# Optimization experiments

Hardware: AMD Instinct MI355X
Metric: run time of the kernel (lower is better)

Reference implementation:

```python
import jax, jax.numpy as jnp
import numpy as np

EPS = 1e-5

def _conv1x1_bn(x, W, b, g, beta):
    # 1x1 conv == channel matmul; BN in training mode uses batch stats over (N,H,W)
    y = jnp.einsum('bchw,oc->bohw', x, W) + b[None, :, None, None]
    mu = jnp.mean(y, axis=(0, 2, 3))
    var = jnp.var(y, axis=(0, 2, 3))
    y = (y - mu[None, :, None, None]) * jax.lax.rsqrt(var + EPS)[None, :, None, None]
    return y * g[None, :, None, None] + beta[None, :, None, None]


def setup_inputs() -> dict:
    key = jax.random.key(0)
    ks = jax.random.split(key, 7)
    b, c, h, w = 8, 256, 64, 64
    sc = 1.0 / np.sqrt(c)
    inp = {
        'x': jax.random.normal(ks[0], (b, c, h, w), jnp.float32),
        'Wq': jax.random.normal(ks[1], (c, c), jnp.float32) * sc,
        'bq': jax.random.normal(ks[2], (c,), jnp.float32) * 0.02,
        'gq': jnp.ones((c,), jnp.float32),
        'betaq': jnp.zeros((c,), jnp.float32),
        'Wk': jax.random.normal(ks[3], (c, c), jnp.float32) * sc,
        'bk': jax.random.normal(ks[4], (c,), jnp.float32) * 0.02,
        'gk': jnp.ones((c,), jnp.float32),
        'betak': jnp.zeros((c,), jnp.float32),
        'Wv': jax.random.normal(ks[5], (c, c), jnp.float32) * sc,
        'bv': jax.random.normal(ks[6], (c,), jnp.float32) * 0.02,
        'gv': jnp.ones((c,), jnp.float32),
        'betav': jnp.zeros((c,), jnp.float32),
    }
    return inp


def reference(x, Wq, bq, gq, betaq, Wk, bk, gk, betak, Wv, bv, gv, betav):
    b, c, h, w = x.shape
    scale = float(h) ** (-0.5)
    Q = _conv1x1_bn(x, Wq, bq, gq, betaq).reshape(b, c, h * w)
    K = _conv1x1_bn(x, Wk, bk, gk, betak).reshape(b, c, h * w)
    V = _conv1x1_bn(x, Wv, bv, gv, betav).reshape(b, c, h * w)
    # un-normalized attention (no softmax)
    pixelMap = jnp.einsum('bcq,bck->bqk', Q, K) * scale  # [b, N, N]
    out = jnp.einsum('bqk,bck->bcq', pixelMap, V)        # [b, c, N]
    return out.reshape(b, c, h, w)
```

## Files before the change

### kernel.cpp

```cpp
#include <hip/hip_runtime.h>
#include <hip/hip_bf16.h>


#define BB 8
#define CC 256
#define NPIX 4096
#define PTOT 32768
#define EPSV 1e-5f
#define SCALEV 0.125f

#define OFF_PG    0L
#define OFF_SP    3145728L
#define OFF_S     3162112L
#define OFF_GHAT  3164160L
#define OFF_XBAR  3229696L
#define OFF_WP    3229952L
#define OFF_WKTF  3426560L
#define OFF_WVTF  3492096L
#define OFF_CVEC  3557632L
#define OFF_U     3558400L
#define OFF_W2    3560448L
#define OFF_HB    3562496L
#define OFF_Y     3564544L
#define OFF_R     3564800L
#define OFF_OFFV  3565056L
#define OFF_GBF   3567104L
#define OFF_WQT   3829248L
#define OFF_WKT   3862016L
#define OFF_WVB   3894784L
#define OFF_ZT    3927552L
#define OFF_FT    3960320L
#define OFF_TBF   4222464L

typedef __attribute__((ext_vector_type(8))) short short8;
typedef __attribute__((ext_vector_type(4))) float f32x4;

#define MFMA16(a, b, c) __builtin_amdgcn_mfma_f32_16x16x32_bf16((a), (b), (c), 0, 0, 0)

__device__ __forceinline__ ushort f2bf(float f) {
    union { float f; unsigned u; } v; v.f = f;
    const unsigned r = (v.u + 0x7FFFu + ((v.u >> 16) & 1u)) >> 16;
    return (ushort)r;
}

__device__ __forceinline__ float bf2f(ushort u) {
    union { unsigned u; float f; } v; v.u = ((unsigned)u) << 16;
    return v.f;
}

__device__ __forceinline__ ushort2 f2bf2(float a, float b) {
    __hip_bfloat162 h = __float22bfloat162_rn(float2{a, b});
    union { __hip_bfloat162 h; ushort2 u; } v; v.h = h;
    return v.u;
}

__device__ __forceinline__ float block_reduce(float v, float* red, int tid) {
    red[tid] = v; __syncthreads();
    for (int st = 128; st > 0; st >>= 1) {
        if (tid < st) red[tid] += red[tid + st];
        __syncthreads();
    }
    float r = red[0]; __syncthreads();
    return r;
}

__global__ __launch_bounds__(256) void gram_mfma(const float* __restrict__ x,
                                                 float* __restrict__ Pg,
                                                 float* __restrict__ Sp) {
    __shared__ __align__(16) ushort Ab[128 * 72];
    __shared__ __align__(16) ushort Bb[128 * 72];
    __shared__ float rs[128];
    const int tid = threadIdx.x;
    const int ks = blockIdx.x, b = blockIdx.y, tt = blockIdx.z;
    const int it = (tt == 1) ? 1 : 0;
    const int jt = (tt == 0) ? 0 : 1;
    const bool diag = (tt < 2);
    const int i0 = it * 128, j0 = jt * 128, k0 = ks * 512;
    const float* xb = x + (long)b * CC * NPIX;
    const int c = tid & 15, rp = tid >> 4;
    const int wave = tid >> 6, lane = tid & 63;
    const int wr = (wave >> 1) * 64, wc = (wave & 1) * 64;
    const int m = lane & 15, q8 = (lane >> 4) * 8;

    if (tid < 128) rs[tid] = 0.f;
    float rloc[8] = {};
    f32x4 acc[4][4];
    #pragma unroll
    for (int a = 0; a < 4; ++a)
        #pragma unroll
        for (int q = 0; q < 4; ++q) acc[a][q] = (f32x4){0.f, 0.f, 0.f, 0.f};

    for (int kc = 0; kc < 512; kc += 64) {
        __syncthreads();
        #pragma unroll
        for (int pp = 0; pp < 8; ++pp) {
            const int row = pp * 16 + rp;
            const float4 v = *(const float4*)&xb[(long)(i0 + row) * NPIX + k0 + kc + c * 4];
            rloc[pp] += v.x + v.y + v.z + v.w;
            const ushort2 w01 = f2bf2(v.x, v.y);
            const ushort2 w23 = f2bf2(v.z, v.w);
            ushort4 w; w.x = w01.x; w.y = w01.y; w.z = w23.x; w.w = w23.y;
            *(ushort4*)&Ab[row * 72 + c * 4] = w;
        }
        if (!diag) {
            #pragma unroll
            for (int pp = 0; pp < 8; ++pp) {
                const int row = pp * 16 + rp;
                const float4 v = *(const float4*)&xb[(long)(j0 + row) * NPIX + k0 + kc + c * 4];
                const ushort2 w01 = f2bf2(v.x, v.y);
                const ushort2 w23 = f2bf2(v.z, v.w);
                ushort4 w; w.x = w01.x; w.y = w01.y; w.z = w23.x; w.w = w23.y;
                *(ushort4*)&Bb[row * 72 + c * 4] = w;
            }
        }
        __syncthreads();
        const ushort* Bsrc = diag ? Ab : Bb;
        #pragma unroll
        for (int kk = 0; kk < 2; ++kk) {
            short8 af[4], bfv[4];
            #pragma unroll
            for (int a = 0; a < 4; ++a)
                af[a] = *(const short8*)&Ab[(wr + a * 16 + m) * 72 + kk * 32 + q8];
            #pragma unroll
            for (int q = 0; q < 4; ++q)
                bfv[q] = *(const short8*)&Bsrc[(wc + q * 16 + m) * 72 + kk * 32 + q8];
            #pragma unroll
            for (int a = 0; a < 4; ++a)
                #pragma unroll
                for (int q = 0; q < 4; ++q)
                    acc[a][q] = MFMA16(af[a], bfv[q], acc[a][q]);
        }
    }
    if (diag) {
        #pragma unroll
        for (int pp = 0; pp < 8; ++pp) atomicAdd(&rs[pp * 16 + rp], rloc[pp]);
        __syncthreads();
        if (tid < 128) Sp[(((long)ks * 8 + b) * 2 + it) * 128 + tid] = rs[tid];
    }
    float* Pt = Pg + (((long)ks * 8 + b) * 3 + tt) * 16384;
    const int rq = (lane >> 4) * 4;
    #pragma unroll
    for (int a = 0; a < 4; ++a) {
        #pragma unroll
        for (int q = 0; q < 4; ++q) {
            const int col = wc + q * 16 + m;
            #pragma unroll
            for (int reg = 0; reg < 4; ++reg)
                Pt[(long)(wr + a * 16 + rq + reg) * 128 + col] = acc[a][q][reg];
        }
    }
}

__global__ __launch_bounds__(256) void reduce_mirror(const float* __restrict__ Pg,
                                                     const float* __restrict__ Sp,
                                                     ushort* __restrict__ Gbf,
                                                     float* __restrict__ Ghat,
                                                     float* __restrict__ S,
                                                     float* __restrict__ xbar) {
    const int blk = blockIdx.x, tid = threadIdx.x;
    if (blk == 48) {
        const int it2 = tid >> 7, rr = tid & 127;
        float xacc = 0.f;
        for (int b = 0; b < BB; ++b) {
            float acc = 0.f;
            #pragma unroll
            for (int ks = 0; ks < 8; ++ks)
                acc += Sp[(((long)ks * 8 + b) * 2 + it2) * 128 + rr];
            S[b * 256 + tid] = acc;
            xacc += acc;
        }
        xbar[tid] = xacc * (1.0f / PTOT);
        return;
    }
    __shared__ float tile[32][33];
    const int tt = blk >> 4, sub = blk & 15;
    const int sr = (sub >> 2) * 32, sc = (sub & 3) * 32;
    const int it = (tt == 1) ? 1 : 0;
    const int jt = (tt == 0) ? 0 : 1;
    const bool offd = (tt == 2);
    const int gi0 = it * 128 + sr, gj0 = jt * 128 + sc;
    const int r = tid >> 3, c4 = (tid & 7) * 4;
    float gh[4] = {0.f, 0.f, 0.f, 0.f};
    for (int b = 0; b < BB; ++b) {
        float s0 = 0.f, s1 = 0.f, s2 = 0.f, s3 = 0.f;
        #pragma unroll
        for (int ks = 0; ks < 8; ++ks) {
            const float4 v = *(const float4*)&Pg[(((long)ks * 8 + b) * 3 + tt) * 16384
                                                 + (long)(sr + r) * 128 + sc + c4];
            s0 += v.x; s1 += v.y; s2 += v.z; s3 += v.w;
        }
        ushort4 w;
        w.x = f2bf(s0); w.y = f2bf(s1); w.z = f2bf(s2); w.w = f2bf(s3);
        *(ushort4*)&Gbf[(long)b * 65536 + (long)(gi0 + r) * 256 + gj0 + c4] = w;
        gh[0] += s0; gh[1] += s1; gh[2] += s2; gh[3] += s3;
        if (offd) {
            tile[r][c4 + 0] = s0; tile[r][c4 + 1] = s1;
            tile[r][c4 + 2] = s2; tile[r][c4 + 3] = s3;
            __syncthreads();
            ushort4 t;
            t.x = f2bf(tile[c4 + 0][r]); t.y = f2bf(tile[c4 + 1][r]);
            t.z = f2bf(tile[c4 + 2][r]); t.w = f2bf(tile[c4 + 3][r]);
            *(ushort4*)&Gbf[(long)b * 65536 + (long)(gj0 + r) * 256 + gi0 + c4] = t;
            __syncthreads();
        }
    }
    float4 g4;
    g4.x = gh[0] * (1.0f / PTOT); g4.y = gh[1] * (1.0f / PTOT);
    g4.z = gh[2] * (1.0f / PTOT); g4.w = gh[3] * (1.0f / PTOT);
    *(float4*)&Ghat[(long)(gi0 + r) * 256 + gj0 + c4] = g4;
    if (offd) {
        tile[r][c4 + 0] = g4.x; tile[r][c4 + 1] = g4.y;
        tile[r][c4 + 2] = g4.z; tile[r][c4 + 3] = g4.w;
        __syncthreads();
        float4 t4;
        t4.x = tile[c4 + 0][r]; t4.y = tile[c4 + 1][r];
        t4.z = tile[c4 + 2][r]; t4.w = tile[c4 + 3][r];
        *(float4*)&Ghat[(long)(gj0 + r) * 256 + gi0 + c4] = t4;
    }
}

__global__ void stats_quad(const float* __restrict__ Wq, const float* __restrict__ Wk,
                           const float* __restrict__ Wv, const float* __restrict__ Ghat,
                           const float* __restrict__ xbar,
                           const float* bq, const float* gq, const float* betaq,
                           const float* bk, const float* gk, const float* betak,
                           const float* bv, const float* gv, const float* betav,
                           float* __restrict__ Wp, float* __restrict__ cvec,
                           ushort* __restrict__ WqT, ushort* __restrict__ WkT,
                           ushort* __restrict__ Wvb, float* __restrict__ WkTf,
                           float* __restrict__ WvTf) {
    const int o = blockIdx.x, t = blockIdx.y, tid = threadIdx.x;
    const float* Wt  = t == 0 ? Wq : (t == 1 ? Wk : Wv);
    const float* bt  = t == 0 ? bq : (t == 1 ? bk : bv);
    const float* gt  = t == 0 ? gq : (t == 1 ? gk : gv);
    const float* bet = t == 0 ? betaq : (t == 1 ? betak : betav);
    __shared__ float wrow[256];
    __shared__ float red[256];
    wrow[tid] = Wt[o * 256 + tid];
    __syncthreads();
    const float* grow = Ghat + (long)tid * 256;
    float tj = 0.f;
    #pragma unroll 8
    for (int k = 0; k < 256; k += 4) {
        const float4 g = *(const float4*)&grow[k];
        tj += g.x * wrow[k] + g.y * wrow[k + 1] + g.z * wrow[k + 2] + g.w * wrow[k + 3];
    }
    const float q2 = block_reduce(wrow[tid] * tj, red, tid);
    const float wx = block_reduce(wrow[tid] * xbar[tid], red, tid);
    const float bo = bt[o];
    const float mu = wx + bo;
    const float var = q2 + 2.f * bo * mu - bo * bo - mu * mu;
    const float a = gt[o] * rsqrtf(var + EPSV);
    const float wpv = a * wrow[tid];
    Wp[(long)t * 65536 + o * 256 + tid] = wpv;
    const ushort wb = f2bf(wpv);
    if (t == 0) {
        WqT[(long)tid * 256 + o] = wb;
    } else if (t == 1) {
        WkT[(long)tid * 256 + o] = wb;
        WkTf[(long)tid * 256 + o] = wpv;
    } else {
        Wvb[(long)o * 256 + tid] = wb;
        WvTf[(long)tid * 256 + o] = wpv;
    }
    if (tid == 0) cvec[t * 256 + o] = a * (bo - mu) + bet[o];
}

__device__ __forceinline__ void gemm_tile(const ushort* __restrict__ Ab,
                                          const ushort* __restrict__ Bb,
                                          ushort* __restrict__ Db,
                                          int m0, int n0, int mode, int bz,
                                          const float* __restrict__ u,
                                          const float* __restrict__ cvec,
                                          const float* __restrict__ r,
                                          const float* __restrict__ hb, int tid) {
    const int wave = tid >> 6, lane = tid & 63;
    const int wr = (wave >> 1) * 64, wc = (wave & 1) * 64;
    const int m = lane & 15, q8 = (lane >> 4) * 8;
    f32x4 acc[4][4];
    #pragma unroll
    for (int a = 0; a < 4; ++a)
        #pragma unroll
        for (int q = 0; q < 4; ++q) acc[a][q] = (f32x4){0.f, 0.f, 0.f, 0.f};
    #pragma unroll
    for (int kk = 0; kk < 8; ++kk) {
        short8 af[4], bfv[4];
        #pragma unroll
        for (int a = 0; a < 4; ++a)
            af[a] = *(const short8*)&Ab[(long)(m0 + wr + a * 16 + m) * 256 + kk * 32 + q8];
        #pragma unroll
        for (int q = 0; q < 4; ++q)
            bfv[q] = *(const short8*)&Bb[(long)(n0 + wc + q * 16 + m) * 256 + kk * 32 + q8];
        #pragma unroll
        for (int a = 0; a < 4; ++a)
            #pragma unroll
            for (int q = 0; q < 4; ++q)
                acc[a][q] = MFMA16(af[a], bfv[q], acc[a][q]);
    }
    const int rq = (lane >> 4) * 4;
    #pragma unroll
    for (int a = 0; a < 4; ++a) {
        #pragma unroll
        for (int q = 0; q < 4; ++q) {
            const int col = n0 + wc + q * 16 + m;
            #pragma unroll
            for (int reg = 0; reg < 4; ++reg) {
                const int row = m0 + wr + a * 16 + rq + reg;
                const float v = acc[a][q][reg];
                if (mode == 0) {
                    Db[(long)col * 256 + row] = f2bf(v);
                } else {
                    const float rv = r[col];
                    const float t2 = hb[bz * 256 + col] + 4096.0f * rv;
                    const float val = SCALEV * (v + u[bz * 256 + row] * rv + cvec[512 + row] * t2);
                    Db[(long)row * 256 + col] = f2bf(val);
                }
            }
        }
    }
}

__global__ __launch_bounds__(256) void zmida(const ushort* __restrict__ WkT,
                                             const ushort* __restrict__ WqT,
                                             ushort* __restrict__ ZT,
                                             const float* __restrict__ Wp,
                                             const float* __restrict__ WkTf,
                                             const float* __restrict__ WvTf,
                                             const float* __restrict__ S,
                                             const float* __restrict__ cvec,
                                             float* __restrict__ u, float* __restrict__ w,
                                             float* __restrict__ y, float* __restrict__ r) {
    const int blk = blockIdx.x, tid = threadIdx.x;
    if (blk < 4) {
        gemm_tile(WkT, WqT, ZT, (blk >> 1) * 128, (blk & 1) * 128, 0, 0,
                  nullptr, nullptr, nullptr, nullptr, tid);
        return;
    }
    const int bidx = blk - 4;
    if (bidx < 8) {
        __shared__ float sh[256];
        sh[tid] = S[bidx * 256 + tid]; __syncthreads();
        float uu = 0.f, ww = 0.f;
        #pragma unroll 8
        for (int j = 0; j < 256; ++j) {
            uu += WvTf[(long)j * 256 + tid] * sh[j];
            ww += WkTf[(long)j * 256 + tid] * sh[j];
        }
        u[bidx * 256 + tid] = uu;
        w[bidx * 256 + tid] = ww;
    } else {
        __shared__ float cqs[256], cks[256];
        cqs[tid] = cvec[tid]; cks[tid] = cvec[256 + tid]; __syncthreads();
        float yy = 0.f, rr = 0.f;
        #pragma unroll 8
        for (int o = 0; o < 256; ++o) {
            yy += Wp[65536L + (long)o * 256 + tid] * cqs[o];
            rr += Wp[(long)o * 256 + tid] * cks[o];
        }
        y[tid] = yy;
        r[tid] = rr;
    }
}

__global__ __launch_bounds__(256) void bcF(const float* __restrict__ Wp,
                                           const ushort* __restrict__ Gbf,
                                           const float* __restrict__ WvTf,
                                           const float* __restrict__ w,
                                           const float* __restrict__ y,
                                           const float* __restrict__ u,
                                           const float* __restrict__ cvec,
                                           float* __restrict__ hb,
                                           float* __restrict__ offv,
                                           const ushort* __restrict__ ZT,
                                           ushort* __restrict__ FT) {
    const int blk = blockIdx.x, tid = threadIdx.x;
    if (blk >= 8) {
        const int idx = blk - 8;
        const int bz = idx >> 2, t = idx & 3;
        gemm_tile(Gbf + (long)bz * 65536, ZT, FT + (long)bz * 65536,
                  (t >> 1) * 128, (t & 1) * 128, 0, 0,
                  nullptr, nullptr, nullptr, nullptr, tid);
        return;
    }
    const int b = blk;
    __shared__ float wl[256], yl[256], gyl[256], red[256], cqs[256], cks[256];
    wl[tid] = w[b * 256 + tid];
    yl[tid] = y[tid];
    cqs[tid] = cvec[tid];
    cks[tid] = cvec[256 + tid];
    const float cv = cvec[512 + tid];
    const float uu = u[b * 256 + tid];
    __syncthreads();
    float hh = 0.f, gg = 0.f;
    #pragma unroll 8
    for (int o = 0; o < 256; ++o) {
        hh += Wp[(long)o * 256 + tid] * wl[o];
        gg += bf2f(Gbf[(long)b * 65536 + (long)o * 256 + tid]) * yl[o];
    }
    hb[b * 256 + tid] = hh;
    gyl[tid] = gg;
    __syncthreads();
    float vg = 0.f;
    #pragma unroll 8
    for (int j = 0; j < 256; ++j) vg += WvTf[(long)j * 256 + tid] * gyl[j];
    const float dkq = block_reduce(cqs[tid] * cks[tid], red, tid);
    const float dwq = block_reduce(wl[tid] * cqs[tid], red, tid);
    offv[b * 256 + tid] = SCALEV * (vg + uu * dkq + cv * (dwq + 4096.0f * dkq));
}

__global__ __launch_bounds__(256) void gemm_T(const ushort* __restrict__ Wvb,
                                              const ushort* __restrict__ FT,
                                              ushort* __restrict__ Tbf,
                                              const float* __restrict__ u,
                                              const float* __restrict__ cvec,
                                              const float* __restrict__ r,
                                              const float* __restrict__ hb) {
    const int bz = blockIdx.z;
    gemm_tile(Wvb, FT + (long)bz * 65536, Tbf + (long)bz * 65536,
              blockIdx.y * 128, blockIdx.x * 128, 1, bz, u, cvec, r, hb, threadIdx.x);
}

__global__ __launch_bounds__(256) void out_mfma(const ushort* __restrict__ Tbf,
                                                const float* __restrict__ x,
                                                const float* __restrict__ offv,
                                                float* __restrict__ out) {
    __shared__ __align__(16) ushort Bs[64 * 264];
    const int tid = threadIdx.x;
    const int p0 = blockIdx.x * 64;
    const int b = blockIdx.y;
    const float* xb = x + (long)b * CC * NPIX;
    const ushort* Tb = Tbf + (long)b * 65536;

    const int c = tid & 15, kq = tid >> 4;
    #pragma unroll
    for (int kt = 0; kt < 4; ++kt) {
        const int k4 = kt * 64 + kq * 4;
        const int p = c * 4;
        const float4 v0 = *(const float4*)&xb[(long)(k4 + 0) * NPIX + p0 + p];
        const float4 v1 = *(const float4*)&xb[(long)(k4 + 1) * NPIX + p0 + p];
        const float4 v2 = *(const float4*)&xb[(long)(k4 + 2) * NPIX + p0 + p];
        const float4 v3 = *(const float4*)&xb[(long)(k4 + 3) * NPIX + p0 + p];
        ushort2 a01, a23;
        ushort4 w;
        a01 = f2bf2(v0.x, v1.x); a23 = f2bf2(v2.x, v3.x);
        w.x = a01.x; w.y = a01.y; w.z = a23.x; w.w = a23.y;
        *(ushort4*)&Bs[(p + 0) * 264 + k4] = w;
        a01 = f2bf2(v0.y, v1.y); a23 = f2bf2(v2.y, v3.y);
        w.x = a01.x; w.y = a01.y; w.z = a23.x; w.w = a23.y;
        *(ushort4*)&Bs[(p + 1) * 264 + k4] = w;
        a01 = f2bf2(v0.z, v1.z); a23 = f2bf2(v2.z, v3.z);
        w.x = a01.x; w.y = a01.y; w.z = a23.x; w.w = a23.y;
        *(ushort4*)&Bs[(p + 2) * 264 + k4] = w;
        a01 = f2bf2(v0.w, v1.w); a23 = f2bf2(v2.w, v3.w);
        w.x = a01.x; w.y = a01.y; w.z = a23.x; w.w = a23.y;
        *(ushort4*)&Bs[(p + 3) * 264 + k4] = w;
    }
    __syncthreads();

    const int wave = tid >> 6, lane = tid & 63;
    const int wr = wave * 64;
    const int m = lane & 15, q8 = (lane >> 4) * 8;
    f32x4 acc[4][4];
    #pragma unroll
    for (int a = 0; a < 4; ++a)
        #pragma unroll
        for (int q = 0; q < 4; ++q) acc[a][q] = (f32x4){0.f, 0.f, 0.f, 0.f};

    #pragma unroll
    for (int kk = 0; kk < 8; ++kk) {
        short8 af[4], bfv[4];
        #pragma unroll
        for (int a = 0; a < 4; ++a)
            af[a] = *(const short8*)&Tb[(long)(wr + a * 16 + m) * 256 + kk * 32 + q8];
        #pragma unroll
        for (int q = 0; q < 4; ++q)
            bfv[q] = *(const short8*)&Bs[(q * 16 + m) * 264 + kk * 32 + q8];
        #pragma unroll
        for (int a = 0; a < 4; ++a)
            #pragma unroll
            for (int q = 0; q < 4; ++q)
                acc[a][q] = MFMA16(af[a], bfv[q], acc[a][q]);
    }

    const int rq = (lane >> 4) * 4;
    #pragma unroll
    for (int a = 0; a < 4; ++a) {
        #pragma unroll
        for (int reg = 0; reg < 4; ++reg) {
            const int row = wr + a * 16 + rq + reg;
            const float off_ = offv[b * CC + row];
            float* orow = &out[((long)b * CC + row) * NPIX + p0];
            #pragma unroll
            for (int q = 0; q < 4; ++q)
                orow[q * 16 + m] = acc[a][q][reg] + off_;
        }
    }
}

extern "C" void kernel_launch(void* const* d_in, const int* in_sizes, int n_in,
                              void* d_out, int out_size, void* d_ws, size_t ws_size,
                              hipStream_t stream) {
    const float* x     = (const float*)d_in[0];
    const float* Wq    = (const float*)d_in[1];
    const float* bq    = (const float*)d_in[2];
    const float* gq    = (const float*)d_in[3];
    const float* betaq = (const float*)d_in[4];
    const float* Wk    = (const float*)d_in[5];
    const float* bk    = (const float*)d_in[6];
    const float* gk    = (const float*)d_in[7];
    const float* betak = (const float*)d_in[8];
    const float* Wv    = (const float*)d_in[9];
    const float* bv    = (const float*)d_in[10];
    const float* gv    = (const float*)d_in[11];
    const float* betav = (const float*)d_in[12];
    float* ws = (float*)d_ws;

    float*  Pg   = ws + OFF_PG;
    float*  Sp   = ws + OFF_SP;
    float*  S    = ws + OFF_S;
    float*  Ghat = ws + OFF_GHAT;
    float*  Xbar = ws + OFF_XBAR;
    float*  Wp   = ws + OFF_WP;
    float*  WkTf = ws + OFF_WKTF;
    float*  WvTf = ws + OFF_WVTF;
    float*  cvec = ws + OFF_CVEC;
    float*  U    = ws + OFF_U;
    float*  W2   = ws + OFF_W2;
    float*  Hb   = ws + OFF_HB;
    float*  Y    = ws + OFF_Y;
    float*  R    = ws + OFF_R;
    float*  OffV = ws + OFF_OFFV;
    ushort* Gbf  = (ushort*)(ws + OFF_GBF);
    ushort* WqT  = (ushort*)(ws + OFF_WQT);
    ushort* WkT  = (ushort*)(ws + OFF_WKT);
    ushort* Wvb  = (ushort*)(ws + OFF_WVB);
    ushort* ZT   = (ushort*)(ws + OFF_ZT);
    ushort* FT   = (ushort*)(ws + OFF_FT);
    ushort* Tbf  = (ushort*)(ws + OFF_TBF);

    gram_mfma<<<dim3(8, 8, 3), 256, 0, stream>>>(x, Pg, Sp);
    reduce_mirror<<<49, 256, 0, stream>>>(Pg, Sp, Gbf, Ghat, S, Xbar);
    stats_quad<<<dim3(256, 3), 256, 0, stream>>>(Wq, Wk, Wv, Ghat, Xbar,
                                                 bq, gq, betaq, bk, gk, betak,
                                                 bv, gv, betav, Wp, cvec,
                                                 WqT, WkT, Wvb, WkTf, WvTf);
    zmida<<<13, 256, 0, stream>>>(WkT, WqT, ZT, Wp, WkTf, WvTf, S, cvec, U, W2, Y, R);
    bcF<<<40, 256, 0, stream>>>(Wp, Gbf, WvTf, W2, Y, U, cvec, Hb, OffV, ZT, FT);
    gemm_T<<<dim3(2, 2, 8), 256, 0, stream>>>(Wvb, FT, Tbf, U, cvec, R, Hb);
    out_mfma<<<dim3(64, 8), 256, 0, stream>>>(Tbf, x, OffV, (float*)d_out);
}
```

Before: 212.9 us.

## Prefetch gram tiles, parallelize reduce over batch with atomics, batch stats rows

The gram kernel now software-prefetches the next 64-column chunk of x into registers while the current chunk is converted and multiplied, and it also zeroes Ghat so that Ghat can be accumulated. reduce_mirror is split across batch, growing from 49 blocks to 385, and accumulates Ghat with atomicAdd instead of looping over batches serially. stats_quad handles four output rows per block with a shuffle-based paired reduction, cutting block count and barrier-heavy reductions. The costs are more registers in the gram kernel, atomic contention on Ghat, and a float summation order that is no longer deterministic.

```diff
diff --git a/kernel.cpp b/kernel.cpp
--- a/kernel.cpp
+++ b/kernel.cpp
@@ -64,14 +64,34 @@
     return r;
 }
 
+__device__ __forceinline__ float2 wred2(float a, float b, float* red8, int tid) {
+    #pragma unroll
+    for (int s = 32; s > 0; s >>= 1) {
+        a += __shfl_xor(a, s);
+        b += __shfl_xor(b, s);
+    }
+    if ((tid & 63) == 0) { red8[(tid >> 6) * 2] = a; red8[(tid >> 6) * 2 + 1] = b; }
+    __syncthreads();
+    const float ra = red8[0] + red8[2] + red8[4] + red8[6];
+    const float rb = red8[1] + red8[3] + red8[5] + red8[7];
+    __syncthreads();
+    return float2{ra, rb};
+}
+
 __global__ __launch_bounds__(256) void gram_mfma(const float* __restrict__ x,
                                                  float* __restrict__ Pg,
-                                                 float* __restrict__ Sp) {
+                                                 float* __restrict__ Sp,
+                                                 float* __restrict__ Ghat) {
     __shared__ __align__(16) ushort Ab[128 * 72];
     __shared__ __align__(16) ushort Bb[128 * 72];
     __shared__ float rs[128];
     const int tid = threadIdx.x;
     const int ks = blockIdx.x, b = blockIdx.y, tt = blockIdx.z;
+    const int lb = (tt * 8 + b) * 8 + ks;
+    if (lb < 64) {
+        #pragma unroll
+        for (int i = 0; i < 4; ++i) Ghat[lb * 1024 + i * 256 + tid] = 0.f;
+    }
     const int it = (tt == 1) ? 1 : 0;
     const int jt = (tt == 0) ? 0 : 1;
     const bool diag = (tt < 2);
@@ -90,12 +110,25 @@
         #pragma unroll
         for (int q = 0; q < 4; ++q) acc[a][q] = (f32x4){0.f, 0.f, 0.f, 0.f};
 
+    const float* Abase = xb + (long)i0 * NPIX + k0 + c * 4;
+    const float* Bbase = xb + (long)j0 * NPIX + k0 + c * 4;
+
+    float4 va[8], vb[8];
+    #pragma unroll
+    for (int pp = 0; pp < 8; ++pp)
+        va[pp] = *(const float4*)&Abase[(long)(pp * 16 + rp) * NPIX];
+    if (!diag) {
+        #pragma unroll
+        for (int pp = 0; pp < 8; ++pp)
+            vb[pp] = *(const float4*)&Bbase[(long)(pp * 16 + rp) * NPIX];
+    }
+
     for (int kc = 0; kc < 512; kc += 64) {
         __syncthreads();
         #pragma unroll
         for (int pp = 0; pp < 8; ++pp) {
             const int row = pp * 16 + rp;
-            const float4 v = *(const float4*)&xb[(long)(i0 + row) * NPIX + k0 + kc + c * 4];
+            const float4 v = va[pp];
             rloc[pp] += v.x + v.y + v.z + v.w;
             const ushort2 w01 = f2bf2(v.x, v.y);
             const ushort2 w23 = f2bf2(v.z, v.w);
@@ -106,11 +139,22 @@
             #pragma unroll
             for (int pp = 0; pp < 8; ++pp) {
                 const int row = pp * 16 + rp;
-                const float4 v = *(const float4*)&xb[(long)(j0 + row) * NPIX + k0 + kc + c * 4];
+                const float4 v = vb[pp];
                 const ushort2 w01 = f2bf2(v.x, v.y);
                 const ushort2 w23 = f2bf2(v.z, v.w);
                 ushort4 w; w.x = w01.x; w.y = w01.y; w.z = w23.x; w.w = w23.y;
                 *(ushort4*)&Bb[row * 72 + c * 4] = w;
+            }
+        }
+        const int kn = kc + 64;
+        if (kn < 512) {
+            #pragma unroll
+            for (int pp = 0; pp < 8; ++pp)
+                va[pp] = *(const float4*)&Abase[(long)(pp * 16 + rp) * NPIX + kn];
+            if (!diag) {
+                #pragma unroll
+                for (int pp = 0; pp < 8; ++pp)
+                    vb[pp] = *(const float4*)&Bbase[(long)(pp * 16 + rp) * NPIX + kn];
             }
         }
         __syncthreads();
@@ -158,7 +202,7 @@
                                                      float* __restrict__ S,
                                                      float* __restrict__ xbar) {
     const int blk = blockIdx.x, tid = threadIdx.x;
-    if (blk == 48) {
+    if (blk == 384) {
         const int it2 = tid >> 7, rr = tid & 127;
         float xacc = 0.f;
         for (int b = 0; b < BB; ++b) {
@@ -173,53 +217,50 @@
         return;
     }
     __shared__ float tile[32][33];
-    const int tt = blk >> 4, sub = blk & 15;
+    const int tt = blk >> 7;
+    const int sub = (blk >> 3) & 15;
+    const int b = blk & 7;
     const int sr = (sub >> 2) * 32, sc = (sub & 3) * 32;
     const int it = (tt == 1) ? 1 : 0;
     const int jt = (tt == 0) ? 0 : 1;
     const bool offd = (tt == 2);
     const int gi0 = it * 128 + sr, gj0 = jt * 128 + sc;
     const int r = tid >> 3, c4 = (tid & 7) * 4;
-    float gh[4] = {0.f, 0.f, 0.f, 0.f};
-    for (int b = 0; b < BB; ++b) {
-        float s0 = 0.f, s1 = 0.f, s2 = 0.f, s3 = 0.f;
-        #pragma unroll
-        for (int ks = 0; ks < 8; ++ks) {
-            const float4 v = *(const float4*)&Pg[(((long)ks * 8 + b) * 3 + tt) * 16384
-                                                 + (long)(sr + r) * 128 + sc + c4];
-            s0 += v.x; s1 += v.y; s2 += v.z; s3 += v.w;
-        }
-        ushort4 w;
-        w.x = f2bf(s0); w.y = f2bf(s1); w.z = f2bf(s2); w.w = f2bf(s3);
-        *(ushort4*)&Gbf[(long)b * 65536 + (long)(gi0 + r) * 256 + gj0 + c4] = w;
-        gh[0] += s0; gh[1] += s1; gh[2] += s2; gh[3] += s3;
-        if (offd) {
-            tile[r][c4 + 0] = s0; tile[r][c4 + 1] = s1;
-            tile[r][c4 + 2] = s2; tile[r][c4 + 3] = s3;
-            __syncthreads();
-            ushort4 t;
-            t.x = f2bf(tile[c4 + 0][r]); t.y = f2bf(tile[c4 + 1][r]);
-            t.z = f2bf(tile[c4 + 2][r]); t.w = f2bf(tile[c4 + 3][r]);
-            *(ushort4*)&Gbf[(long)b * 65536 + (long)(gj0 + r) * 256 + gi0 + c4] = t;
-            __syncthreads();
-        }
-    }
-    float4 g4;
-    g4.x = gh[0] * (1.0f / PTOT); g4.y = gh[1] * (1.0f / PTOT);
-    g4.z = gh[2] * (1.0f / PTOT); g4.w = gh[3] * (1.0f / PTOT);
-    *(float4*)&Ghat[(long)(gi0 + r) * 256 + gj0 + c4] = g4;
+    const float inv = 1.0f / PTOT;
+
+    float s0 = 0.f, s1 = 0.f, s2 = 0.f, s3 = 0.f;
+    #pragma unroll
+    for (int ks = 0; ks < 8; ++ks) {
+        const float4 v = *(const float4*)&Pg[(((long)ks * 8 + b) * 3 + tt) * 16384
+                                             + (long)(sr + r) * 128 + sc + c4];
+        s0 += v.x; s1 += v.y; s2 += v.z; s3 += v.w;
+    }
+    ushort4 w;
+    w.x = f2bf(s0); w.y = f2bf(s1); w.z = f2bf(s2); w.w = f2bf(s3);
+    *(ushort4*)&Gbf[(long)b * 65536 + (long)(gi0 + r) * 256 + gj0 + c4] = w;
+    float* gd = &Ghat[(long)(gi0 + r) * 256 + gj0 + c4];
+    atomicAdd(gd + 0, s0 * inv);
+    atomicAdd(gd + 1, s1 * inv);
+    atomicAdd(gd + 2, s2 * inv);
+    atomicAdd(gd + 3, s3 * inv);
     if (offd) {
-        tile[r][c4 + 0] = g4.x; tile[r][c4 + 1] = g4.y;
-        tile[r][c4 + 2] = g4.z; tile[r][c4 + 3] = g4.w;
+        tile[r][c4 + 0] = s0; tile[r][c4 + 1] = s1;
+        tile[r][c4 + 2] = s2; tile[r][c4 + 3] = s3;
         __syncthreads();
-        float4 t4;
-        t4.x = tile[c4 + 0][r]; t4.y = tile[c4 + 1][r];
-        t4.z = tile[c4 + 2][r]; t4.w = tile[c4 + 3][r];
-        *(float4*)&Ghat[(long)(gj0 + r) * 256 + gi0 + c4] = t4;
-    }
-}
-
-__global__ void stats_quad(const float* __restrict__ Wq, const float* __restrict__ Wk,
+        const float t0 = tile[c4 + 0][r], t1 = tile[c4 + 1][r];
+        const float t2 = tile[c4 + 2][r], t3 = tile[c4 + 3][r];
+        ushort4 tw;
+        tw.x = f2bf(t0); tw.y = f2bf(t1); tw.z = f2bf(t2); tw.w = f2bf(t3);
+        *(ushort4*)&Gbf[(long)b * 65536 + (long)(gj0 + r) * 256 + gi0 + c4] = tw;
+        float* gm = &Ghat[(long)(gj0 + r) * 256 + gi0 + c4];
+        atomicAdd(gm + 0, t0 * inv);
+        atomicAdd(gm + 1, t1 * inv);
+        atomicAdd(gm + 2, t2 * inv);
+        atomicAdd(gm + 3, t3 * inv);
+    }
+}
+
+__global__ __launch_bounds__(256) void stats_quad(const float* __restrict__ Wq, const float* __restrict__ Wk,
                            const float* __restrict__ Wv, const float* __restrict__ Ghat,
                            const float* __restrict__ xbar,
                            const float* bq, const float* gq, const float* betaq,
@@ -229,41 +270,51 @@
                            ushort* __restrict__ WqT, ushort* __restrict__ WkT,
                            ushort* __restrict__ Wvb, float* __restrict__ WkTf,
                            float* __restrict__ WvTf) {
-    const int o = blockIdx.x, t = blockIdx.y, tid = threadIdx.x;
+    const int og = blockIdx.x, t = blockIdx.y, tid = threadIdx.x;
+    const int o0 = og * 4;
     const float* Wt  = t == 0 ? Wq : (t == 1 ? Wk : Wv);
     const float* bt  = t == 0 ? bq : (t == 1 ? bk : bv);
     const float* gt  = t == 0 ? gq : (t == 1 ? gk : gv);
     const float* bet = t == 0 ? betaq : (t == 1 ? betak : betav);
-    __shared__ float wrow[256];
-    __shared__ float red[256];
-    wrow[tid] = Wt[o * 256 + tid];
+    __shared__ float wrows[4][256];
+    __shared__ float red8[8];
+    #pragma unroll
+    for (int i = 0; i < 4; ++i) wrows[i][tid] = Wt[(o0 + i) * 256 + tid];
+    const float xb = xbar[tid];
     __syncthreads();
     const float* grow = Ghat + (long)tid * 256;
-    float tj = 0.f;
+    float tj[4] = {0.f, 0.f, 0.f, 0.f};
     #pragma unroll 8
     for (int k = 0; k < 256; k += 4) {
         const float4 g = *(const float4*)&grow[k];
-        tj += g.x * wrow[k] + g.y * wrow[k + 1] + g.z * wrow[k + 2] + g.w * wrow[k + 3];
-    }
-    const float q2 = block_reduce(wrow[tid] * tj, red, tid);
-    const float wx = block_reduce(wrow[tid] * xbar[tid], red, tid);
-    const float bo = bt[o];
-    const float mu = wx + bo;
-    const float var = q2 + 2.f * bo * mu - bo * bo - mu * mu;
-    const float a = gt[o] * rsqrtf(var + EPSV);
-    const float wpv = a * wrow[tid];
-    Wp[(long)t * 65536 + o * 256 + tid] = wpv;
-    const ushort wb = f2bf(wpv);
-    if (t == 0) {
-        WqT[(long)tid * 256 + o] = wb;
-    } else if (t == 1) {
-        WkT[(long)tid * 256 + o] = wb;
-        WkTf[(long)tid * 256 + o] = wpv;
-    } else {
-        Wvb[(long)o * 256 + tid] = wb;
-        WvTf[(long)tid * 256 + o] = wpv;
-    }
-    if (tid == 0) cvec[t * 256 + o] = a * (bo - mu) + bet[o];
+        #pragma unroll
+        for (int i = 0; i < 4; ++i)
+            tj[i] += g.x * wrows[i][k]     + g.y * wrows[i][k + 1]
+                   + g.z * wrows[i][k + 2] + g.w * wrows[i][k + 3];
+    }
+    #pragma unroll
+    for (int i = 0; i < 4; ++i) {
+        const int o = o0 + i;
+        const float wv = wrows[i][tid];
+        const float2 qw = wred2(wv * tj[i], wv * xb, red8, tid);
+        const float bo = bt[o];
+        const float mu = qw.y + bo;
+        const float var = qw.x + 2.f * bo * mu - bo * bo - mu * mu;
+        const float a = gt[o] * rsqrtf(var + EPSV);
+        const float wpv = a * wv;
+        Wp[(long)t * 65536 + o * 256 + tid] = wpv;
+        const ushort wb = f2bf(wpv);
+        if (t == 0) {
+            WqT[(long)tid * 256 + o] = wb;
+        } else if (t == 1) {
+            WkT[(long)tid * 256 + o] = wb;
+            WkTf[(long)tid * 256 + o] = wpv;
+        } else {
+            Wvb[(long)o * 256 + tid] = wb;
+            WvTf[(long)tid * 256 + o] = wpv;
+        }
+        if (tid == 0) cvec[t * 256 + o] = a * (bo - mu) + bet[o];
+    }
 }
 
 __device__ __forceinline__ void gemm_tile(const ushort* __restrict__ Ab,
@@ -538,12 +589,12 @@
     ushort* FT   = (ushort*)(ws + OFF_FT);
     ushort* Tbf  = (ushort*)(ws + OFF_TBF);
 
-    gram_mfma<<<dim3(8, 8, 3), 256, 0, stream>>>(x, Pg, Sp);
-    reduce_mirror<<<49, 256, 0, stream>>>(Pg, Sp, Gbf, Ghat, S, Xbar);
-    stats_quad<<<dim3(256, 3), 256, 0, stream>>>(Wq, Wk, Wv, Ghat, Xbar,
-                                                 bq, gq, betaq, bk, gk, betak,
-                                                 bv, gv, betav, Wp, cvec,
-                                                 WqT, WkT, Wvb, WkTf, WvTf);
+    gram_mfma<<<dim3(8, 8, 3), 256, 0, stream>>>(x, Pg, Sp, Ghat);
+    reduce_mirror<<<385, 256, 0, stream>>>(Pg, Sp, Gbf, Ghat, S, Xbar);
+    stats_quad<<<dim3(64, 3), 256, 0, stream>>>(Wq, Wk, Wv, Ghat, Xbar,
+                                                bq, gq, betaq, bk, gk, betak,
+                                                bv, gv, betav, Wp, cvec,
+                                                WqT, WkT, Wvb, WkTf, WvTf);
     zmida<<<13, 256, 0, stream>>>(WkT, WqT, ZT, Wp, WkTf, WvTf, S, cvec, U, W2, Y, R);
     bcF<<<40, 256, 0, stream>>>(Wp, Gbf, WvTf, W2, Y, U, cvec, Hb, OffV, ZT, FT);
     gemm_T<<<dim3(2, 2, 8), 256, 0, stream>>>(Wvb, FT, Tbf, U, cvec, R, Hb);
```

New measurement: 197.7 us. -7.1%, faster.
